# Kernel tuning notes

Measured on AMD Instinct MI355X. Metric: run time of the kernel, lower is better.

## Reference

```python
import jax, jax.numpy as jnp
import numpy as np

N = 50000      # nodes
E = 200000     # edges (before self-loops)
HID = 64       # hidden_channels
HEADS = 8
VOCAB = 100    # node-type vocabulary for the embedding
NEG_SLOPE = 0.2
EPS = 1e-16


def _gatv2(x, src, dst, Wl, bl, Wr, br, att, bias, heads, out_ch):
    """GATv2Conv (PyG defaults: share_weights=False, concat=True, neg_slope=0.2).
    x: [N, F_in]; src/dst: [E_tot] (self-loops already appended).
    Returns [N, heads*out_ch]."""
    n = x.shape[0]
    xl = (x @ Wl + bl).reshape(n, heads, out_ch)   # source transform
    xr = (x @ Wr + br).reshape(n, heads, out_ch)   # target transform
    m = xl[src] + xr[dst]                          # [E, H, C]
    e = jnp.einsum('ehc,hc->eh', jax.nn.leaky_relu(m, NEG_SLOPE), att)  # [E, H]
    # segment softmax over incoming edges of each destination node
    e_max = jax.ops.segment_max(e, dst, num_segments=n)
    e_exp = jnp.exp(e - e_max[dst])
    denom = jax.ops.segment_sum(e_exp, dst, num_segments=n)
    alpha = e_exp / (denom[dst] + EPS)             # [E, H]
    out = jax.ops.segment_sum(alpha[:, :, None] * xl[src], dst, num_segments=n)
    return out.reshape(n, heads * out_ch) + bias


def setup_inputs() -> dict:
    key = jax.random.key(0)
    ks = jax.random.split(key, 16)
    s = 0.1
    return {
        'x': jax.random.randint(ks[0], (N,), 0, VOCAB),
        'edge_index': jax.random.randint(ks[1], (2, E), 0, N),
        'emb': jax.random.normal(ks[2], (VOCAB, HID), dtype=jnp.float32) * s,
        'Wl1': jax.random.normal(ks[3], (HID, HEADS * HID), dtype=jnp.float32) * s,
        'bl1': jnp.zeros((HEADS * HID,), jnp.float32),
        'Wr1': jax.random.normal(ks[4], (HID, HEADS * HID), dtype=jnp.float32) * s,
        'br1': jnp.zeros((HEADS * HID,), jnp.float32),
        'att1': jax.random.normal(ks[5], (HEADS, HID), dtype=jnp.float32) * s,
        'bias1': jnp.zeros((HEADS * HID,), jnp.float32),
        'Wl2': jax.random.normal(ks[6], (HEADS * HID, 2), dtype=jnp.float32) * s,
        'bl2': jnp.zeros((2,), jnp.float32),
        'Wr2': jax.random.normal(ks[7], (HEADS * HID, 2), dtype=jnp.float32) * s,
        'br2': jnp.zeros((2,), jnp.float32),
        'att2': jax.random.normal(ks[8], (1, 2), dtype=jnp.float32) * s,
        'bias2': jnp.zeros((2,), jnp.float32),
    }


def reference(x, edge_index, emb, Wl1, bl1, Wr1, br1, att1, bias1,
              Wl2, bl2, Wr2, br2, att2, bias2):
    # PyG GATv2Conv adds self-loops by default
    loops = jnp.arange(N, dtype=edge_index.dtype)
    src = jnp.concatenate([edge_index[0], loops])
    dst = jnp.concatenate([edge_index[1], loops])

    h = emb[x]                                       # embedding lookup [N, HID]
    # dropout layers are identity in eval mode
    h = _gatv2(h, src, dst, Wl1, bl1, Wr1, br1, att1, bias1, HEADS, HID)
    h = jax.nn.elu(h)
    out = _gatv2(h, src, dst, Wl2, bl2, Wr2, br2, att2, bias2, 1, 2)
    return out                                       # [N, 2]
```

## Files before the change

### kernel.cpp

```cpp
#include <hip/hip_runtime.h>
#include <hip/hip_fp16.h>
#include <math.h>

#define NEG_SLOPE 0.2f
#define EPSV 1e-16f
#define CAP 32

struct __align__(16) h8v { __half2 a, b, c, d; };

__global__ __launch_bounds__(256) void kA_tables_fill(
    const float* __restrict__ emb, const float* __restrict__ Wl1,
    const float* __restrict__ bl1, const float* __restrict__ Wr1,
    const float* __restrict__ br1,
    const int* __restrict__ srcE, const int* __restrict__ dstE,
    const int* __restrict__ x,
    float* __restrict__ table_l, float* __restrict__ table_r,
    __half* __restrict__ table_lh,
    int* __restrict__ cnt, int* __restrict__ adj,
    int nb_tab, int nb_E, int E, int N, int VOCAB, int tshift)
{
    int b = blockIdx.x;
    if (b < nb_tab) {
        int idx = b * 256 + threadIdx.x;
        if (idx < VOCAB * 512) {
            int t = idx >> 9, o = idx & 511;
            float sl = bl1[o], sr = br1[o];
            const float* e = emb + t * 64;
            #pragma unroll 8
            for (int k = 0; k < 64; ++k) {
                float ev = e[k];
                sl = fmaf(ev, Wl1[k * 512 + o], sl);
                sr = fmaf(ev, Wr1[k * 512 + o], sr);
            }
            table_l[idx] = sl;
            table_r[idx] = sr;
            table_lh[idx] = __float2half_rn(sl);
        }
    } else if (b < nb_tab + nb_E) {
        int e = (b - nb_tab) * 256 + threadIdx.x;
        if (e < E) {
            int d = dstE[e];
            int sv = srcE[e];
            int pos = 1 + atomicAdd(&cnt[d], 1);
            if (pos < CAP) adj[d * CAP + pos] = (sv << tshift) | x[sv];
        }
    } else {
        int d = (b - nb_tab - nb_E) * 256 + threadIdx.x;
        if (d < N) adj[d * CAP] = (d << tshift) | x[d];
    }
}

__global__ __launch_bounds__(256) void kB_epair(
    const float* __restrict__ table_l, const float* __restrict__ table_r,
    const float* __restrict__ att1, float* __restrict__ exp_pair, int VOCAB)
{
    int idx = blockIdx.x * 256 + threadIdx.x;
    if (idx >= VOCAB * VOCAB * 8) return;
    int h = idx & 7;
    int p = idx >> 3;
    int ts = p % VOCAB;
    int td = p / VOCAB;
    const float4* tl = (const float4*)(table_l + ts * 512 + h * 64);
    const float4* tr = (const float4*)(table_r + td * 512 + h * 64);
    const float4* a  = (const float4*)(att1 + h * 64);
    float s = 0.f;
    #pragma unroll
    for (int c4 = 0; c4 < 16; ++c4) {
        float4 l = tl[c4], r = tr[c4], av = a[c4];
        float m0 = l.x + r.x; m0 = m0 > 0.f ? m0 : NEG_SLOPE * m0; s = fmaf(m0, av.x, s);
        float m1 = l.y + r.y; m1 = m1 > 0.f ? m1 : NEG_SLOPE * m1; s = fmaf(m1, av.y, s);
        float m2 = l.z + r.z; m2 = m2 > 0.f ? m2 : NEG_SLOPE * m2; s = fmaf(m2, av.z, s);
        float m3 = l.w + r.w; m3 = m3 > 0.f ? m3 : NEG_SLOPE * m3; s = fmaf(m3, av.w, s);
    }
    exp_pair[idx] = __expf(s);
}

__global__ __launch_bounds__(256, 4) void k4_node_agg(
    const int* __restrict__ x, const int* __restrict__ cnt,
    const int* __restrict__ adj,
    const __half* __restrict__ table_lh, const float* __restrict__ exp_pair,
    const float* __restrict__ bias1,
    const float* __restrict__ Wl2, const float* __restrict__ bl2,
    const float* __restrict__ Wr2, const float* __restrict__ br2,
    float2* __restrict__ xl2, float2* __restrict__ xr2,
    int N, int VOCAB, int tmask)
{
    int wid = __builtin_amdgcn_readfirstlane(blockIdx.x * 4 + (threadIdx.x >> 6));
    if (wid >= N) return;
    int lane = threadIdx.x & 63;
    int hc = lane >> 3;

    const int* arow = adj + wid * CAP;
    int4 A0 = ((const int4*)arow)[0];
    int4 A1 = ((const int4*)arow)[1];
    int deg = min(cnt[wid], CAP - 1) + 1;
    int td = x[wid];
    const float* ep = exp_pair + (size_t)td * (VOCAB * 8);

    int ts[8];
    ts[0] = A0.x & tmask; ts[1] = A0.y & tmask;
    ts[2] = A0.z & tmask; ts[3] = A0.w & tmask;
    ts[4] = A1.x & tmask; ts[5] = A1.y & tmask;
    ts[6] = A1.z & tmask; ts[7] = A1.w & tmask;
    int ts0 = ts[0];
    #pragma unroll
    for (int e = 1; e < 8; ++e) if (e >= deg) ts[e] = ts0;

    float we[8];
    #pragma unroll
    for (int e = 0; e < 8; ++e) we[e] = ep[ts[e] * 8 + hc];
    h8v hv[8];
    #pragma unroll
    for (int e = 0; e < 8; ++e)
        hv[e] = *(const h8v*)(table_lh + (size_t)ts[e] * 512 + lane * 8);

    float sw = 0.f;
    float acc[8] = {0.f, 0.f, 0.f, 0.f, 0.f, 0.f, 0.f, 0.f};
    #pragma unroll
    for (int e = 0; e < 8; ++e) {
        float w = (e < deg) ? we[e] : 0.f;
        sw += w;
        float2 f0 = __half22float2(hv[e].a);
        float2 f1 = __half22float2(hv[e].b);
        float2 f2 = __half22float2(hv[e].c);
        float2 f3 = __half22float2(hv[e].d);
        acc[0] = fmaf(w, f0.x, acc[0]); acc[1] = fmaf(w, f0.y, acc[1]);
        acc[2] = fmaf(w, f1.x, acc[2]); acc[3] = fmaf(w, f1.y, acc[3]);
        acc[4] = fmaf(w, f2.x, acc[4]); acc[5] = fmaf(w, f2.y, acc[5]);
        acc[6] = fmaf(w, f3.x, acc[6]); acc[7] = fmaf(w, f3.y, acc[7]);
    }
    for (int base = 8; base < deg; base += 4) {
        int t4[4];
        #pragma unroll
        for (int u = 0; u < 4; ++u) {
            int e = base + u;
            t4[u] = ((e < deg) ? arow[e] : arow[0]) & tmask;
        }
        float w4[4];
        #pragma unroll
        for (int u = 0; u < 4; ++u) w4[u] = ep[t4[u] * 8 + hc];
        h8v g4[4];
        #pragma unroll
        for (int u = 0; u < 4; ++u)
            g4[u] = *(const h8v*)(table_lh + (size_t)t4[u] * 512 + lane * 8);
        #pragma unroll
        for (int u = 0; u < 4; ++u) {
            float w = (base + u < deg) ? w4[u] : 0.f;
            sw += w;
            float2 f0 = __half22float2(g4[u].a);
            float2 f1 = __half22float2(g4[u].b);
            float2 f2 = __half22float2(g4[u].c);
            float2 f3 = __half22float2(g4[u].d);
            acc[0] = fmaf(w, f0.x, acc[0]); acc[1] = fmaf(w, f0.y, acc[1]);
            acc[2] = fmaf(w, f1.x, acc[2]); acc[3] = fmaf(w, f1.y, acc[3]);
            acc[4] = fmaf(w, f2.x, acc[4]); acc[5] = fmaf(w, f2.y, acc[5]);
            acc[6] = fmaf(w, f3.x, acc[6]); acc[7] = fmaf(w, f3.y, acc[7]);
        }
    }
    float inv_dn = 1.f / (sw + EPSV);

    const float4* b4 = (const float4*)(bias1 + lane * 8);
    float4 b0 = b4[0], b1 = b4[1];
    float bb[8] = {b0.x, b0.y, b0.z, b0.w, b1.x, b1.y, b1.z, b1.w};
    float h1[8];
    #pragma unroll
    for (int j = 0; j < 8; ++j) {
        float v = fmaf(acc[j], inv_dn, bb[j]);
        h1[j] = v > 0.f ? v : (__expf(v) - 1.f);
    }
    const float4* wl4 = (const float4*)(Wl2 + lane * 16);
    const float4* wr4 = (const float4*)(Wr2 + lane * 16);
    float sl0 = 0.f, sl1 = 0.f, sr0 = 0.f, sr1 = 0.f;
    #pragma unroll
    for (int k = 0; k < 4; ++k) {
        float4 vl = wl4[k], vr = wr4[k];
        float ha = h1[2 * k], hb = h1[2 * k + 1];
        sl0 = fmaf(ha, vl.x, sl0); sl1 = fmaf(ha, vl.y, sl1);
        sl0 = fmaf(hb, vl.z, sl0); sl1 = fmaf(hb, vl.w, sl1);
        sr0 = fmaf(ha, vr.x, sr0); sr1 = fmaf(ha, vr.y, sr1);
        sr0 = fmaf(hb, vr.z, sr0); sr1 = fmaf(hb, vr.w, sr1);
    }
    #pragma unroll
    for (int mm = 1; mm < 64; mm <<= 1) {
        sl0 += __shfl_xor(sl0, mm);
        sl1 += __shfl_xor(sl1, mm);
        sr0 += __shfl_xor(sr0, mm);
        sr1 += __shfl_xor(sr1, mm);
    }
    if (lane == 0) {
        xl2[wid] = make_float2(sl0 + bl2[0], sl1 + bl2[1]);
        xr2[wid] = make_float2(sr0 + br2[0], sr1 + br2[1]);
    }
}

__global__ __launch_bounds__(256) void k5_layer2(
    const int* __restrict__ cnt, const int* __restrict__ adj,
    const float2* __restrict__ xl2, const float2* __restrict__ xr2,
    const float* __restrict__ att2, const float* __restrict__ bias2,
    float2* __restrict__ out, int N, int tshift)
{
    int wid = blockIdx.x * 4 + (threadIdx.x >> 6);
    int lane = threadIdx.x & 63;
    int g = lane >> 3, j = lane & 7;
    int d = wid * 8 + g;
    int dc = min(d, N - 1);
    int start = dc * CAP;
    float a0 = att2[0], a1 = att2[1];

    int aw = adj[start + j];
    int deg = min(cnt[dc], CAP - 1) + 1;
    float2 xr = xr2[dc];
    int src = min(aw >> tshift, N - 1);
    float2 xl = xl2[src];
    float m0 = xl.x + xr.x; m0 = m0 > 0.f ? m0 : NEG_SLOPE * m0;
    float m1 = xl.y + xr.y; m1 = m1 > 0.f ? m1 : NEG_SLOPE * m1;
    float ev = fmaf(a0, m0, a1 * m1);
    float w = (j < deg) ? __expf(ev) : 0.f;
    float s = w, o0 = w * xl.x, o1 = w * xl.y;

    for (int e = j + 8; e < deg; e += 8) {
        int src2 = min(adj[start + e] >> tshift, N - 1);
        float2 x2 = xl2[src2];
        float n0 = x2.x + xr.x; n0 = n0 > 0.f ? n0 : NEG_SLOPE * n0;
        float n1 = x2.y + xr.y; n1 = n1 > 0.f ? n1 : NEG_SLOPE * n1;
        float e2 = fmaf(a0, n0, a1 * n1);
        float w2 = __expf(e2);
        s += w2;
        o0 = fmaf(w2, x2.x, o0);
        o1 = fmaf(w2, x2.y, o1);
    }
    #pragma unroll
    for (int off = 1; off < 8; off <<= 1) {
        s  += __shfl_xor(s, off);
        o0 += __shfl_xor(o0, off);
        o1 += __shfl_xor(o1, off);
    }
    if (d < N && j == 0) {
        float inv = 1.f / (s + EPSV);
        out[d] = make_float2(fmaf(o0, inv, bias2[0]), fmaf(o1, inv, bias2[1]));
    }
}

extern "C" void kernel_launch(void* const* d_in, const int* in_sizes, int n_in,
                              void* d_out, int out_size, void* d_ws, size_t ws_size,
                              hipStream_t stream) {
    (void)n_in; (void)out_size; (void)ws_size;
    const int*   x     = (const int*)d_in[0];
    const int*   ei    = (const int*)d_in[1];
    const float* emb   = (const float*)d_in[2];
    const float* Wl1   = (const float*)d_in[3];
    const float* bl1   = (const float*)d_in[4];
    const float* Wr1   = (const float*)d_in[5];
    const float* br1   = (const float*)d_in[6];
    const float* att1  = (const float*)d_in[7];
    const float* bias1 = (const float*)d_in[8];
    const float* Wl2   = (const float*)d_in[9];
    const float* bl2   = (const float*)d_in[10];
    const float* Wr2   = (const float*)d_in[11];
    const float* br2   = (const float*)d_in[12];
    const float* att2  = (const float*)d_in[13];
    const float* bias2 = (const float*)d_in[14];
    float* out = (float*)d_out;

    int N = in_sizes[0];
    int E = in_sizes[1] / 2;
    int VOCAB = in_sizes[2] / 64;
    const int* srcE = ei;
    const int* dstE = ei + E;

    int tshift = 1;
    while ((1 << tshift) < VOCAB) ++tshift;
    int tmask = (1 << tshift) - 1;

    float*  table_l  = (float*)d_ws;
    float*  table_r  = table_l + (size_t)VOCAB * 512;
    float*  exp_pair = table_r + (size_t)VOCAB * 512;
    __half* table_lh = (__half*)(exp_pair + (size_t)VOCAB * VOCAB * 8);
    int*    cnt      = (int*)(table_lh + (size_t)VOCAB * 512);
    int*    adj      = cnt + ((N + 3) & ~3);
    float*  xl2      = (float*)(adj + (size_t)N * CAP);
    float*  xr2      = xl2 + 2 * (size_t)N;

    hipMemsetAsync(cnt, 0, sizeof(int) * (size_t)N, stream);

    int nb_tab = (VOCAB * 512 + 255) / 256;
    int nb_E = (E + 255) / 256;
    int nb_N = (N + 255) / 256;

    kA_tables_fill<<<nb_tab + nb_E + nb_N, 256, 0, stream>>>(
        emb, Wl1, bl1, Wr1, br1, srcE, dstE, x,
        table_l, table_r, table_lh, cnt, adj, nb_tab, nb_E, E, N, VOCAB, tshift);

    int nb_ep = (VOCAB * VOCAB * 8 + 255) / 256;
    kB_epair<<<nb_ep, 256, 0, stream>>>(table_l, table_r, att1, exp_pair, VOCAB);

    k4_node_agg<<<(N + 3) / 4, 256, 0, stream>>>(
        x, cnt, adj, table_lh, exp_pair, bias1, Wl2, bl2, Wr2, br2,
        (float2*)xl2, (float2*)xr2, N, VOCAB, tmask);

    k5_layer2<<<(N + 31) / 32, 256, 0, stream>>>(
        cnt, adj, (const float2*)xl2, (const float2*)xr2,
        att2, bias2, (float2*)out, N, tshift);
}
```

Baseline: 159.9 us.

## Stage fp16 source table in LDS with persistent node-aggregation blocks

The node aggregation kernel becomes a persistent kernel of 256 blocks of 1024 threads. Each block first copies the whole fp16 vocabulary table (100x512 halves, about 100KB) into shared memory, then loops over a contiguous chunk of destination nodes. The per-edge feature gathers now read LDS instead of global or L2. In exchange, occupancy is limited to one large block per CU, every block pays for the table copy plus a barrier, and the table is silently clamped to MAXV entries.

```diff
diff --git a/kernel.cpp b/kernel.cpp
--- a/kernel.cpp
+++ b/kernel.cpp
@@ -5,6 +5,7 @@
 #define NEG_SLOPE 0.2f
 #define EPSV 1e-16f
 #define CAP 32
+#define MAXV 100
 
 struct __align__(16) h8v { __half2 a, b, c, d; };
 
@@ -75,7 +76,7 @@
     exp_pair[idx] = __expf(s);
 }
 
-__global__ __launch_bounds__(256, 4) void k4_node_agg(
+__global__ __launch_bounds__(1024, 1) void k4_node_agg(
     const int* __restrict__ x, const int* __restrict__ cnt,
     const int* __restrict__ adj,
     const __half* __restrict__ table_lh, const float* __restrict__ exp_pair,
@@ -85,111 +86,128 @@
     float2* __restrict__ xl2, float2* __restrict__ xr2,
     int N, int VOCAB, int tmask)
 {
-    int wid = __builtin_amdgcn_readfirstlane(blockIdx.x * 4 + (threadIdx.x >> 6));
-    if (wid >= N) return;
+    __shared__ __half tab[MAXV * 512];
+    int vcap = min(VOCAB, MAXV);
+    {
+        const int4* s = (const int4*)table_lh;
+        int4* t4p = (int4*)tab;
+        int total = vcap * 64;
+        for (int i = threadIdx.x; i < total; i += 1024) t4p[i] = s[i];
+    }
+    __syncthreads();
+
     int lane = threadIdx.x & 63;
+    int wv = threadIdx.x >> 6;
     int hc = lane >> 3;
 
-    const int* arow = adj + wid * CAP;
-    int4 A0 = ((const int4*)arow)[0];
-    int4 A1 = ((const int4*)arow)[1];
-    int deg = min(cnt[wid], CAP - 1) + 1;
-    int td = x[wid];
-    const float* ep = exp_pair + (size_t)td * (VOCAB * 8);
-
-    int ts[8];
-    ts[0] = A0.x & tmask; ts[1] = A0.y & tmask;
-    ts[2] = A0.z & tmask; ts[3] = A0.w & tmask;
-    ts[4] = A1.x & tmask; ts[5] = A1.y & tmask;
-    ts[6] = A1.z & tmask; ts[7] = A1.w & tmask;
-    int ts0 = ts[0];
-    #pragma unroll
-    for (int e = 1; e < 8; ++e) if (e >= deg) ts[e] = ts0;
-
-    float we[8];
-    #pragma unroll
-    for (int e = 0; e < 8; ++e) we[e] = ep[ts[e] * 8 + hc];
-    h8v hv[8];
-    #pragma unroll
-    for (int e = 0; e < 8; ++e)
-        hv[e] = *(const h8v*)(table_lh + (size_t)ts[e] * 512 + lane * 8);
-
-    float sw = 0.f;
-    float acc[8] = {0.f, 0.f, 0.f, 0.f, 0.f, 0.f, 0.f, 0.f};
-    #pragma unroll
-    for (int e = 0; e < 8; ++e) {
-        float w = (e < deg) ? we[e] : 0.f;
-        sw += w;
-        float2 f0 = __half22float2(hv[e].a);
-        float2 f1 = __half22float2(hv[e].b);
-        float2 f2 = __half22float2(hv[e].c);
-        float2 f3 = __half22float2(hv[e].d);
-        acc[0] = fmaf(w, f0.x, acc[0]); acc[1] = fmaf(w, f0.y, acc[1]);
-        acc[2] = fmaf(w, f1.x, acc[2]); acc[3] = fmaf(w, f1.y, acc[3]);
-        acc[4] = fmaf(w, f2.x, acc[4]); acc[5] = fmaf(w, f2.y, acc[5]);
-        acc[6] = fmaf(w, f3.x, acc[6]); acc[7] = fmaf(w, f3.y, acc[7]);
-    }
-    for (int base = 8; base < deg; base += 4) {
-        int t4[4];
-        #pragma unroll
-        for (int u = 0; u < 4; ++u) {
-            int e = base + u;
-            t4[u] = ((e < deg) ? arow[e] : arow[0]) & tmask;
-        }
-        float w4[4];
-        #pragma unroll
-        for (int u = 0; u < 4; ++u) w4[u] = ep[t4[u] * 8 + hc];
-        h8v g4[4];
-        #pragma unroll
-        for (int u = 0; u < 4; ++u)
-            g4[u] = *(const h8v*)(table_lh + (size_t)t4[u] * 512 + lane * 8);
-        #pragma unroll
-        for (int u = 0; u < 4; ++u) {
-            float w = (base + u < deg) ? w4[u] : 0.f;
-            sw += w;
-            float2 f0 = __half22float2(g4[u].a);
-            float2 f1 = __half22float2(g4[u].b);
-            float2 f2 = __half22float2(g4[u].c);
-            float2 f3 = __half22float2(g4[u].d);
-            acc[0] = fmaf(w, f0.x, acc[0]); acc[1] = fmaf(w, f0.y, acc[1]);
-            acc[2] = fmaf(w, f1.x, acc[2]); acc[3] = fmaf(w, f1.y, acc[3]);
-            acc[4] = fmaf(w, f2.x, acc[4]); acc[5] = fmaf(w, f2.y, acc[5]);
-            acc[6] = fmaf(w, f3.x, acc[6]); acc[7] = fmaf(w, f3.y, acc[7]);
-        }
-    }
-    float inv_dn = 1.f / (sw + EPSV);
+    int chunk = (N + gridDim.x - 1) / gridDim.x;
+    int nd1 = min((int)(blockIdx.x + 1) * chunk, N);
 
     const float4* b4 = (const float4*)(bias1 + lane * 8);
     float4 b0 = b4[0], b1 = b4[1];
     float bb[8] = {b0.x, b0.y, b0.z, b0.w, b1.x, b1.y, b1.z, b1.w};
-    float h1[8];
-    #pragma unroll
-    for (int j = 0; j < 8; ++j) {
-        float v = fmaf(acc[j], inv_dn, bb[j]);
-        h1[j] = v > 0.f ? v : (__expf(v) - 1.f);
-    }
-    const float4* wl4 = (const float4*)(Wl2 + lane * 16);
-    const float4* wr4 = (const float4*)(Wr2 + lane * 16);
-    float sl0 = 0.f, sl1 = 0.f, sr0 = 0.f, sr1 = 0.f;
-    #pragma unroll
-    for (int k = 0; k < 4; ++k) {
-        float4 vl = wl4[k], vr = wr4[k];
-        float ha = h1[2 * k], hb = h1[2 * k + 1];
-        sl0 = fmaf(ha, vl.x, sl0); sl1 = fmaf(ha, vl.y, sl1);
-        sl0 = fmaf(hb, vl.z, sl0); sl1 = fmaf(hb, vl.w, sl1);
-        sr0 = fmaf(ha, vr.x, sr0); sr1 = fmaf(ha, vr.y, sr1);
-        sr0 = fmaf(hb, vr.z, sr0); sr1 = fmaf(hb, vr.w, sr1);
-    }
-    #pragma unroll
-    for (int mm = 1; mm < 64; mm <<= 1) {
-        sl0 += __shfl_xor(sl0, mm);
-        sl1 += __shfl_xor(sl1, mm);
-        sr0 += __shfl_xor(sr0, mm);
-        sr1 += __shfl_xor(sr1, mm);
-    }
-    if (lane == 0) {
-        xl2[wid] = make_float2(sl0 + bl2[0], sl1 + bl2[1]);
-        xr2[wid] = make_float2(sr0 + br2[0], sr1 + br2[1]);
+    int tclamp = vcap - 1;
+
+    for (int d0 = blockIdx.x * chunk + wv; d0 < nd1; d0 += 16) {
+        int wid = __builtin_amdgcn_readfirstlane(d0);
+        const int* arow = adj + wid * CAP;
+        int4 A0 = ((const int4*)arow)[0];
+        int4 A1 = ((const int4*)arow)[1];
+        int deg = min(cnt[wid], CAP - 1) + 1;
+        int td = x[wid];
+        const float* ep = exp_pair + (size_t)td * (VOCAB * 8);
+
+        int ts[8];
+        ts[0] = min(A0.x & tmask, tclamp); ts[1] = min(A0.y & tmask, tclamp);
+        ts[2] = min(A0.z & tmask, tclamp); ts[3] = min(A0.w & tmask, tclamp);
+        ts[4] = min(A1.x & tmask, tclamp); ts[5] = min(A1.y & tmask, tclamp);
+        ts[6] = min(A1.z & tmask, tclamp); ts[7] = min(A1.w & tmask, tclamp);
+        int ts0 = ts[0];
+        #pragma unroll
+        for (int e = 1; e < 8; ++e) if (e >= deg) ts[e] = ts0;
+
+        float we[8];
+        #pragma unroll
+        for (int e = 0; e < 8; ++e) we[e] = ep[ts[e] * 8 + hc];
+        h8v hv[8];
+        #pragma unroll
+        for (int e = 0; e < 8; ++e)
+            hv[e] = *(const h8v*)(tab + ts[e] * 512 + lane * 8);
+
+        float sw = 0.f;
+        float acc[8] = {0.f, 0.f, 0.f, 0.f, 0.f, 0.f, 0.f, 0.f};
+        #pragma unroll
+        for (int e = 0; e < 8; ++e) {
+            float w = (e < deg) ? we[e] : 0.f;
+            sw += w;
+            float2 p0 = __half22float2(hv[e].a);
+            float2 p1 = __half22float2(hv[e].b);
+            float2 p2 = __half22float2(hv[e].c);
+            float2 p3 = __half22float2(hv[e].d);
+            acc[0] = fmaf(w, p0.x, acc[0]); acc[1] = fmaf(w, p0.y, acc[1]);
+            acc[2] = fmaf(w, p1.x, acc[2]); acc[3] = fmaf(w, p1.y, acc[3]);
+            acc[4] = fmaf(w, p2.x, acc[4]); acc[5] = fmaf(w, p2.y, acc[5]);
+            acc[6] = fmaf(w, p3.x, acc[6]); acc[7] = fmaf(w, p3.y, acc[7]);
+        }
+        for (int base = 8; base < deg; base += 4) {
+            int t4i[4];
+            #pragma unroll
+            for (int u = 0; u < 4; ++u) {
+                int e = base + u;
+                t4i[u] = min(((e < deg) ? arow[e] : arow[0]) & tmask, tclamp);
+            }
+            float w4[4];
+            #pragma unroll
+            for (int u = 0; u < 4; ++u) w4[u] = ep[t4i[u] * 8 + hc];
+            h8v g4[4];
+            #pragma unroll
+            for (int u = 0; u < 4; ++u)
+                g4[u] = *(const h8v*)(tab + t4i[u] * 512 + lane * 8);
+            #pragma unroll
+            for (int u = 0; u < 4; ++u) {
+                float w = (base + u < deg) ? w4[u] : 0.f;
+                sw += w;
+                float2 p0 = __half22float2(g4[u].a);
+                float2 p1 = __half22float2(g4[u].b);
+                float2 p2 = __half22float2(g4[u].c);
+                float2 p3 = __half22float2(g4[u].d);
+                acc[0] = fmaf(w, p0.x, acc[0]); acc[1] = fmaf(w, p0.y, acc[1]);
+                acc[2] = fmaf(w, p1.x, acc[2]); acc[3] = fmaf(w, p1.y, acc[3]);
+                acc[4] = fmaf(w, p2.x, acc[4]); acc[5] = fmaf(w, p2.y, acc[5]);
+                acc[6] = fmaf(w, p3.x, acc[6]); acc[7] = fmaf(w, p3.y, acc[7]);
+            }
+        }
+        float inv_dn = 1.f / (sw + EPSV);
+
+        float h1[8];
+        #pragma unroll
+        for (int j = 0; j < 8; ++j) {
+            float v = fmaf(acc[j], inv_dn, bb[j]);
+            h1[j] = v > 0.f ? v : (__expf(v) - 1.f);
+        }
+        const float4* wl4 = (const float4*)(Wl2 + lane * 16);
+        const float4* wr4 = (const float4*)(Wr2 + lane * 16);
+        float sl0 = 0.f, sl1 = 0.f, sr0 = 0.f, sr1 = 0.f;
+        #pragma unroll
+        for (int k = 0; k < 4; ++k) {
+            float4 vl = wl4[k], vr = wr4[k];
+            float ha = h1[2 * k], hb = h1[2 * k + 1];
+            sl0 = fmaf(ha, vl.x, sl0); sl1 = fmaf(ha, vl.y, sl1);
+            sl0 = fmaf(hb, vl.z, sl0); sl1 = fmaf(hb, vl.w, sl1);
+            sr0 = fmaf(ha, vr.x, sr0); sr1 = fmaf(ha, vr.y, sr1);
+            sr0 = fmaf(hb, vr.z, sr0); sr1 = fmaf(hb, vr.w, sr1);
+        }
+        #pragma unroll
+        for (int mm = 1; mm < 64; mm <<= 1) {
+            sl0 += __shfl_xor(sl0, mm);
+            sl1 += __shfl_xor(sl1, mm);
+            sr0 += __shfl_xor(sr0, mm);
+            sr1 += __shfl_xor(sr1, mm);
+        }
+        if (lane == 0) {
+            xl2[wid] = make_float2(sl0 + bl2[0], sl1 + bl2[1]);
+            xr2[wid] = make_float2(sr0 + br2[0], sr1 + br2[1]);
+        }
     }
 }
 
@@ -294,7 +312,7 @@
     int nb_ep = (VOCAB * VOCAB * 8 + 255) / 256;
     kB_epair<<<nb_ep, 256, 0, stream>>>(table_l, table_r, att1, exp_pair, VOCAB);
 
-    k4_node_agg<<<(N + 3) / 4, 256, 0, stream>>>(
+    k4_node_agg<<<256, 1024, 0, stream>>>(
         x, cnt, adj, table_lh, exp_pair, bias1, Wl2, bl2, Wr2, br2,
         (float2*)xl2, (float2*)xr2, N, VOCAB, tmask);
 
```

After: 154.3 us. 1.04x faster.
